# Kernel optimization log

Measured on AMD Instinct MI355X. Metric: run time of the kernel, lower is better.

The kernel has to match this reference:

```python
import jax, jax.numpy as jnp
import numpy as np

B, L, H = 8, 1024, 512
CHUNK = 16  # query-row chunk size for the score computation; L % CHUNK == 0


def setup_inputs() -> dict:
    key = jax.random.key(0)
    ks = jax.random.split(key, 6)
    s = 1.0 / np.sqrt(H)  # torch nn.Linear default init bound
    return {
        "inputs": jax.random.normal(ks[0], (B, L, H), jnp.float32),
        "W1": jax.random.uniform(ks[1], (H, H), jnp.float32, -s, s),
        "b1": jax.random.uniform(ks[2], (H,), jnp.float32, -s, s),
        "W2": jax.random.uniform(ks[3], (H, H), jnp.float32, -s, s),
        "b2": jax.random.uniform(ks[4], (H,), jnp.float32, -s, s),
        # torch: nn.init.normal_(q, mean=-0.02, std=0.02)
        "q": jax.random.normal(ks[5], (H,), jnp.float32) * 0.02 - 0.02,
    }


def _scores(u1, u2, q):
    # u[b,i,j] = tanh(u1[b,i,:] + u2[b,j,:]) . q  -- computed in row-chunks to
    # avoid materializing the full [B,L,L,H] tensor the torch loop implies.
    Bx, Lx, Hx = u1.shape
    n = Lx // CHUNK
    u1c = u1.reshape(Bx, n, CHUNK, Hx).transpose(1, 0, 2, 3)  # [n, B, c, H]

    def step(carry, u1_i):
        t = jnp.tanh(u1_i[:, :, None, :] + u2[:, None, :, :])  # [B, c, L, H]
        return carry, jnp.einsum('bclh,h->bcl', t, q)

    _, s = jax.lax.scan(jax.checkpoint(step), None, u1c)  # [n, B, c, L]
    return s.transpose(1, 0, 2, 3).reshape(Bx, Lx, Lx)


def reference(inputs, W1, b1, W2, b2, q):
    u1 = inputs @ W1.T + b1  # [B, L, H]
    u2 = inputs @ W2.T + b2  # [B, L, H]
    u = _scores(u1, u2, q)   # [B, L, L]
    # relu=False in init, so no relu on u
    a = jax.nn.softmax(u, axis=2)
    h = jnp.einsum('bij,bjh->bih', a, inputs)  # [B, L, H]
    return h, a
```

## Files before the change

kernel.cpp:

```cpp
#include <hip/hip_runtime.h>

typedef _Float16 f16;
typedef _Float16 f16x2 __attribute__((ext_vector_type(2)));
typedef _Float16 f16x4 __attribute__((ext_vector_type(4)));
typedef _Float16 f16x8 __attribute__((ext_vector_type(8)));
typedef float f32x4 __attribute__((ext_vector_type(4)));

#define LOG2E_X2 2.8853900817779268f

__constant__ float D8[8] = {0.543915f, 0.177997f, 0.0652351f, 0.0242575f,
                            0.00903807f, 0.00336823f, 0.00125536f, 0.000467884f};

static __device__ __forceinline__ void gl2lds16(const void* g, void* l) {
  __builtin_amdgcn_global_load_lds((const __attribute__((address_space(1))) void*)g,
                                   (__attribute__((address_space(3))) void*)l, 16, 0, 0);
}


__global__ __launch_bounds__(256) void k_prep_x(const float* __restrict__ X,
                                                f16* __restrict__ Xh, f16* __restrict__ XhT) {
  const int ht = blockIdx.x, it = blockIdx.y, b = blockIdx.z;
  __shared__ f16 Lt[64][72];
  const int t = threadIdx.x;
  const int r = t >> 4, c4 = (t & 15) * 4;
  const float* Xb = X + ((size_t)b * 1024 + it * 64) * 512 + ht * 64;
#pragma unroll
  for (int k = 0; k < 4; ++k) {
    const int rr = r + 16 * k;
    float4 v = *(const float4*)&Xb[(size_t)rr * 512 + c4];
    f16 h0 = (f16)v.x, h1 = (f16)v.y, h2 = (f16)v.z, h3 = (f16)v.w;
    *(f16x4*)&Xh[((size_t)b * 1024 + it * 64 + rr) * 512 + ht * 64 + c4] = {h0, h1, h2, h3};
    Lt[c4 + 0][rr] = h0; Lt[c4 + 1][rr] = h1; Lt[c4 + 2][rr] = h2; Lt[c4 + 3][rr] = h3;
  }
  __syncthreads();
  const int hr = t >> 2, seg = t & 3;
  f16* dst = &XhT[((size_t)b * 512 + ht * 64 + hr) * 1024 + it * 64 + seg * 16];
  *(f16x8*)(dst) = *(const f16x8*)&Lt[hr][seg * 16];
  *(f16x8*)(dst + 8) = *(const f16x8*)&Lt[hr][seg * 16 + 8];
}

__global__ __launch_bounds__(256) void k_prep_w(const float* __restrict__ W1,
                                                const float* __restrict__ W2,
                                                f16* __restrict__ Wh) {
  const int row = blockIdx.x, z = blockIdx.y, t = threadIdx.x;
  const float* W = z ? W2 : W1;
  float2 v = *(const float2*)&W[(size_t)row * 512 + t * 2];
  *(f16x2*)&Wh[(size_t)z * 262144 + (size_t)row * 512 + t * 2] = {(f16)v.x, (f16)v.y};
}

template <int NM>
__global__ __launch_bounds__(256) void k_trig(const float* __restrict__ u1,
                                              const float* __restrict__ u2,
                                              const float* __restrict__ q,
                                              f16* __restrict__ At, f16* __restrict__ Bt,
                                              float* __restrict__ qa, float* __restrict__ qb,
                                              int m0, int wq) {
  const int i = blockIdx.x, t = threadIdx.x;
  const float w = 0.62831853f;
  const float2 a2 = *(const float2*)&u1[(size_t)i * 512 + 2 * t];
  const float2 b2 = *(const float2*)&u2[(size_t)i * 512 + 2 * t];
  const float2 q2 = *(const float2*)&q[2 * t];
  if (wq) {
    float sa = q2.x * a2.x + q2.y * a2.y;
    float sb = q2.x * b2.x + q2.y * b2.y;
#pragma unroll
    for (int o = 1; o < 64; o <<= 1) { sa += __shfl_xor(sa, o); sb += __shfl_xor(sb, o); }
    __shared__ float red[8];
    const int lane = t & 63, widx = t >> 6;
    if (lane == 0) { red[widx] = sa; red[4 + widx] = sb; }
    __syncthreads();
    if (t == 0) qa[i] = red[0] + red[1] + red[2] + red[3];
    if (t == 1) qb[i] = red[4] + red[5] + red[6] + red[7];
  }
  float s1[4], c1[4], sm_[4], cm_[4];
  const float ang[4] = {w * a2.x, w * a2.y, w * b2.x, w * b2.y};
#pragma unroll
  for (int u = 0; u < 4; ++u) {
    __sincosf(ang[u], &s1[u], &c1[u]);
    if (m0 == 1) { sm_[u] = s1[u]; cm_[u] = c1[u]; }
    else __sincosf(m0 * ang[u], &sm_[u], &cm_[u]);
  }
  const size_t ldT = (size_t)NM * 1024;
  f16* Ar = At + (size_t)i * ldT + 2 * t;
  f16* Br = Bt + (size_t)i * ldT + 2 * t;
#pragma unroll
  for (int j = 0; j < NM; ++j) {
    const float dm = D8[m0 - 1 + j];
    const float qdx = q2.x * dm, qdy = q2.y * dm;
    *(f16x2*)(Ar + j * 1024)       = {(f16)(qdx * sm_[0]), (f16)(qdy * sm_[1])};
    *(f16x2*)(Ar + j * 1024 + 512) = {(f16)(qdx * cm_[0]), (f16)(qdy * cm_[1])};
    *(f16x2*)(Br + j * 1024)       = {(f16)cm_[2], (f16)cm_[3]};
    *(f16x2*)(Br + j * 1024 + 512) = {(f16)sm_[2], (f16)sm_[3]};
    if (j + 1 < NM) {
#pragma unroll
      for (int u = 0; u < 4; ++u) {
        const float ns = sm_[u] * c1[u] + cm_[u] * s1[u];
        const float nc = cm_[u] * c1[u] - sm_[u] * s1[u];
        sm_[u] = ns; cm_[u] = nc;
      }
    }
  }
}

template <int MODE, int ACC>
__global__ __launch_bounds__(512, 2) void k_gemm(
    const f16* __restrict__ A, const f16* __restrict__ B, float* __restrict__ C,
    const float* __restrict__ e0, const float* __restrict__ e1,
    int Kloop, int ldAB, long halfA, long halfC) {
  __shared__ alignas(16) char sm[2][2][256 * 64 * 2];
  const int t = threadIdx.x;
  const int nx = blockIdx.x, my = blockIdx.y, z = blockIdx.z;
  const f16* Ab; const f16* Bb; float* Cb; const float* bias = nullptr;
  int ldC;
  if (MODE == 0) {
    Ab = A + (size_t)my * 256 * ldAB;
    Bb = B + (size_t)z * 262144 + (size_t)nx * 256 * ldAB;
    Cb = C + (size_t)z * 4194304 + (size_t)my * 256 * 512 + nx * 256;
    bias = (z ? e1 : e0) + nx * 256;
    ldC = 512;
  } else if (MODE == 1) {
    const int b = z & 7, h = z >> 3;
    Ab = A + ((size_t)(b * 1024 + my * 256)) * ldAB + h * halfA;
    Bb = B + ((size_t)(b * 1024 + nx * 256)) * ldAB + h * halfA;
    Cb = C + h * halfC + ((size_t)(b * 1024 + my * 256)) * 1024 + nx * 256;
    ldC = 1024;
  } else {
    Ab = A + ((size_t)(z * 1024 + my * 256)) * ldAB;
    Bb = B + ((size_t)(z * 512 + nx * 256)) * ldAB;
    Cb = C + (size_t)z * 524288 + (size_t)my * 256 * 512 + nx * 256;
    ldC = 512;
  }
  const int wid = t >> 6, lane = t & 63;
  const int wr = wid >> 2, wc = wid & 3;
  const int rl = lane & 15, kc = lane >> 4;
  f32x4 acc[8][4] = {};

  auto stage = [&](int buf, int kt) {
    const f16* gA = Ab + kt * 64;
    const f16* gB = Bb + kt * 64;
    char* lA = sm[buf][0];
    char* lB = sm[buf][1];
#pragma unroll
    for (int ii = 0; ii < 4; ++ii) {
      const int lin = ii * 512 + t;
      const int row = lin >> 3, c = lin & 7;
      const size_t go = (size_t)row * ldAB + ((c ^ (row & 7)) * 8);
      gl2lds16(gA + go, lA + ii * 8192 + wid * 1024);
      gl2lds16(gB + go, lB + ii * 8192 + wid * 1024);
    }
  };

  const int nkt = Kloop >> 6;
  stage(0, 0);
  __syncthreads();
  for (int kt = 0; kt < nkt; ++kt) {
    const int cur = kt & 1;
    if (kt + 1 < nkt) stage(cur ^ 1, kt + 1);
    const char* lA = sm[cur][0];
    const char* lB = sm[cur][1];
#pragma unroll
    for (int kk = 0; kk < 2; ++kk) {
      f16x8 av[8], bv[4];
#pragma unroll
      for (int fi = 0; fi < 8; ++fi) {
        const int rloc = wr * 128 + fi * 16 + rl;
        av[fi] = *(const f16x8*)(lA + rloc * 128 + (((kc + 4 * kk) ^ (rloc & 7)) << 4));
      }
#pragma unroll
      for (int fj = 0; fj < 4; ++fj) {
        const int cloc = wc * 64 + fj * 16 + rl;
        bv[fj] = *(const f16x8*)(lB + cloc * 128 + (((kc + 4 * kk) ^ (cloc & 7)) << 4));
      }
#pragma unroll
      for (int fi = 0; fi < 8; ++fi)
#pragma unroll
        for (int fj = 0; fj < 4; ++fj)
          acc[fi][fj] = __builtin_amdgcn_mfma_f32_16x16x32_f16(av[fi], bv[fj], acc[fi][fj], 0, 0, 0);
    }
    __syncthreads();
  }
#pragma unroll
  for (int fj = 0; fj < 4; ++fj) {
    const int gcol = wc * 64 + fj * 16 + rl;
    const float bvv = (MODE == 0) ? bias[gcol] : 0.f;
#pragma unroll
    for (int fi = 0; fi < 8; ++fi) {
      const int grow0 = wr * 128 + fi * 16 + kc * 4;
      f32x4 v = acc[fi][fj];
#pragma unroll
      for (int r = 0; r < 4; ++r) {
        const size_t o = (size_t)(grow0 + r) * ldC + gcol;
        float x = v[r] + bvv;
        if (ACC) x += Cb[o];
        Cb[o] = x;
      }
    }
  }
}

__global__ __launch_bounds__(256) void k_softmax2(const float* __restrict__ P0,
                                                  const float* __restrict__ P1,
                                                  const float* __restrict__ qa,
                                                  const float* __restrict__ qb,
                                                  float* __restrict__ out_a,
                                                  f16* __restrict__ a16) {
  const int row = blockIdx.x, t = threadIdx.x;
  const int b = row >> 10;
  const size_t off = (size_t)row * 1024 + t * 4;
  float4 p0 = *(const float4*)(P0 + off);
  float4 p1 = *(const float4*)(P1 + off);
  float4 qb4 = *(const float4*)(qb + (size_t)b * 1024 + t * 4);
  const float qi = qa[row];
  float4 v;
  v.x = p0.x + p1.x + 0.2f * (qi + qb4.x);
  v.y = p0.y + p1.y + 0.2f * (qi + qb4.y);
  v.z = p0.z + p1.z + 0.2f * (qi + qb4.z);
  v.w = p0.w + p1.w + 0.2f * (qi + qb4.w);
  float m = fmaxf(fmaxf(v.x, v.y), fmaxf(v.z, v.w));
#pragma unroll
  for (int o = 1; o < 64; o <<= 1) m = fmaxf(m, __shfl_xor(m, o));
  __shared__ float red[4];
  const int w = t >> 6, ln = t & 63;
  if (ln == 0) red[w] = m;
  __syncthreads();
  m = fmaxf(fmaxf(red[0], red[1]), fmaxf(red[2], red[3]));
  v.x = __expf(v.x - m); v.y = __expf(v.y - m);
  v.z = __expf(v.z - m); v.w = __expf(v.w - m);
  float s = v.x + v.y + v.z + v.w;
#pragma unroll
  for (int o = 1; o < 64; o <<= 1) s += __shfl_xor(s, o);
  __syncthreads();
  if (ln == 0) red[w] = s;
  __syncthreads();
  s = red[0] + red[1] + red[2] + red[3];
  const float inv = 1.0f / s;
  v.x *= inv; v.y *= inv; v.z *= inv; v.w *= inv;
  *(float4*)(out_a + off) = v;
  *(f16x4*)(a16 + off) = {(f16)v.x, (f16)v.y, (f16)v.z, (f16)v.w};
}

typedef short s16x2 __attribute__((ext_vector_type(2)));

static __device__ __forceinline__ float fdot2f(f16x2 a, f16x2 b, float c) {
#if __has_builtin(__builtin_amdgcn_fdot2)
  return __builtin_amdgcn_fdot2(a, b, c, false);
#else
  return c + (float)a[0] * (float)b[0] + (float)a[1] * (float)b[1];
#endif
}

__global__ void k_qprep(const float* __restrict__ q, f16* __restrict__ qh,
                        float* __restrict__ qsum) {
  const int t = threadIdx.x;
  float v = q[t];
  qh[t] = (f16)v;
  float s = v;
#pragma unroll
  for (int o = 1; o < 64; o <<= 1) s += __shfl_xor(s, o);
  __shared__ float red[8];
  if ((t & 63) == 0) red[t >> 6] = s;
  __syncthreads();
  if (t == 0) {
    float tot = 0.f;
#pragma unroll
    for (int i = 0; i < 8; ++i) tot += red[i];
    *qsum = tot;
  }
}

__global__ __launch_bounds__(256) void k_gemm_exp(
    const float* __restrict__ X, const float* __restrict__ W1,
    const float* __restrict__ b1, const float* __restrict__ W2,
    const float* __restrict__ b2, f16* __restrict__ e1, f16* __restrict__ e2) {
  const int z = blockIdx.z;
  const float* W = z ? W2 : W1;
  const float* bias = z ? b2 : b1;
  f16* out = z ? e2 : e1;
  const int r0 = blockIdx.y * 64;
  const int c0 = blockIdx.x * 64;
  __shared__ alignas(16) float Xs[64][68];
  __shared__ alignas(16) float Ws[64][68];
  const int t = threadIdx.x;
  const int row = t >> 2, seg = t & 3;
  const int tr = t >> 4, tc = t & 15;
  float acc[4][4] = {};
#pragma unroll 1
  for (int k0 = 0; k0 < 512; k0 += 64) {
    const float4* gx = (const float4*)(X + (size_t)(r0 + row) * 512 + k0 + seg * 16);
    float4* lx = (float4*)(&Xs[row][seg * 16]);
    lx[0] = gx[0]; lx[1] = gx[1]; lx[2] = gx[2]; lx[3] = gx[3];
    const float4* gw = (const float4*)(W + (size_t)(c0 + row) * 512 + k0 + seg * 16);
    float4* lw = (float4*)(&Ws[row][seg * 16]);
    lw[0] = gw[0]; lw[1] = gw[1]; lw[2] = gw[2]; lw[3] = gw[3];
    __syncthreads();
#pragma unroll 4
    for (int kk = 0; kk < 64; kk += 4) {
      float4 av[4], bv[4];
#pragma unroll
      for (int ii = 0; ii < 4; ++ii) av[ii] = *(const float4*)&Xs[tr + 16 * ii][kk];
#pragma unroll
      for (int jj = 0; jj < 4; ++jj) bv[jj] = *(const float4*)&Ws[tc + 16 * jj][kk];
#pragma unroll
      for (int ii = 0; ii < 4; ++ii) {
#pragma unroll
        for (int jj = 0; jj < 4; ++jj) {
          acc[ii][jj] = fmaf(av[ii].x, bv[jj].x, acc[ii][jj]);
          acc[ii][jj] = fmaf(av[ii].y, bv[jj].y, acc[ii][jj]);
          acc[ii][jj] = fmaf(av[ii].z, bv[jj].z, acc[ii][jj]);
          acc[ii][jj] = fmaf(av[ii].w, bv[jj].w, acc[ii][jj]);
        }
      }
    }
    __syncthreads();
  }
#pragma unroll
  for (int ii = 0; ii < 4; ++ii) {
    const int r = r0 + tr + 16 * ii;
#pragma unroll
    for (int jj = 0; jj < 4; ++jj) {
      const int c = c0 + tc + 16 * jj;
      float u = acc[ii][jj] + bias[c];
      float val = u * LOG2E_X2 - 4.0f;
      val = fminf(6.6759f, fmaxf(-14.6759f, val));
      out[(size_t)r * 512 + c] = (f16)exp2f(val);
    }
  }
}

template <int P>
static __device__ __forceinline__ void tanh_dot_step(const f16x8 (&Av)[4],
                                                     const f16x8 (&Bv)[4],
                                                     const f16x8& Qv, float (&acc)[4][4],
                                                     int c256, int kmag, int two2) {
  f16x2 qp = __builtin_shufflevector(Qv, Qv, 2 * P, 2 * P + 1);
#pragma unroll
  for (int jj = 0; jj < 4; ++jj) {
    f16x2 bp = __builtin_shufflevector(Bv[jj], Bv[jj], 2 * P, 2 * P + 1);
#pragma unroll
    for (int ii = 0; ii < 4; ++ii) {
      f16x2 ap = __builtin_shufflevector(Av[ii], Av[ii], 2 * P, 2 * P + 1);
      f16x2 d, r, tt;
      asm("v_pk_fma_f16 %0, %3, %4, %5\n\t"
          "v_pk_sub_i16 %1, %6, %0\n\t"
          "v_pk_fma_f16 %2, %0, %1, %7 neg_lo:[1,0,0] neg_hi:[1,0,0]\n\t"
          "v_pk_mul_f16 %1, %1, %2\n\t"
          "v_pk_fma_f16 %2, %0, %1, %7 neg_lo:[1,0,0] neg_hi:[1,0,0]\n\t"
          "v_pk_mul_f16 %1, %1, %2"
          : "=&v"(d), "=&v"(r), "=&v"(tt)
          : "v"(ap), "v"(bp), "v"(c256), "v"(kmag), "v"(two2));
      acc[ii][jj] = fdot2f(r, qp, acc[ii][jj]);
    }
  }
}

__global__ __launch_bounds__(256) void k_scores(const f16* __restrict__ e1,
                                                const f16* __restrict__ e2,
                                                const f16* __restrict__ qh,
                                                const float* __restrict__ qsum_p,
                                                float* __restrict__ out_a) {
  const int b = blockIdx.z, it = blockIdx.y, jt = blockIdx.x;
  __shared__ alignas(16) f16 As[64][72];
  __shared__ alignas(16) f16 Bs[64][72];
  __shared__ alignas(16) f16 Qs[512];
  const int t = threadIdx.x;
  const size_t eA = (size_t)(b * 1024 + it * 64) * 512;
  const size_t eB = (size_t)(b * 1024 + jt * 64) * 512;
  if (t < 64) ((uint4*)Qs)[t] = ((const uint4*)qh)[t];
  const int row = t >> 2, seg = t & 3;
  const int tr = t >> 4, tc = t & 15;
  const int c256 = 0x1C001C00;
  const int kmag = 0x77987798;
  const int two2 = 0x40004000;
  float acc[4][4] = {};
#pragma unroll 1
  for (int h0 = 0; h0 < 512; h0 += 64) {
    const f16* gA = e1 + eA + (size_t)row * 512 + h0;
    const f16* gB = e2 + eB + (size_t)row * 512 + h0;
    *(uint4*)(&As[row][seg * 8]) = *(const uint4*)(gA + seg * 8);
    *(uint4*)(&As[row][seg * 8 + 32]) = *(const uint4*)(gA + seg * 8 + 32);
    *(uint4*)(&Bs[row][seg * 8]) = *(const uint4*)(gB + seg * 8);
    *(uint4*)(&Bs[row][seg * 8 + 32]) = *(const uint4*)(gB + seg * 8 + 32);
    __syncthreads();
#pragma unroll 2
    for (int g = 0; g < 8; ++g) {
      f16x8 Av[4], Bv[4], Qv;
#pragma unroll
      for (int ii = 0; ii < 4; ++ii) Av[ii] = *(const f16x8*)&As[tr + 16 * ii][g * 8];
#pragma unroll
      for (int jj = 0; jj < 4; ++jj) Bv[jj] = *(const f16x8*)&Bs[tc + 16 * jj][g * 8];
      Qv = *(const f16x8*)&Qs[h0 + g * 8];
      tanh_dot_step<0>(Av, Bv, Qv, acc, c256, kmag, two2);
      tanh_dot_step<1>(Av, Bv, Qv, acc, c256, kmag, two2);
      tanh_dot_step<2>(Av, Bv, Qv, acc, c256, kmag, two2);
      tanh_dot_step<3>(Av, Bv, Qv, acc, c256, kmag, two2);
    }
    __syncthreads();
  }
  const float qs = *qsum_p;
#pragma unroll
  for (int ii = 0; ii < 4; ++ii) {
    const size_t orow = (size_t)(b * 1024 + it * 64 + tr + 16 * ii) * 1024;
#pragma unroll
    for (int jj = 0; jj < 4; ++jj)
      out_a[orow + jt * 64 + tc + 16 * jj] = qs - acc[ii][jj] * (1.0f / 128.0f);
  }
}

__global__ __launch_bounds__(256) void k_softmax(float* __restrict__ a) {
  float* row = a + (size_t)blockIdx.x * 1024;
  const int t = threadIdx.x;
  float4 v = ((const float4*)row)[t];
  float m = fmaxf(fmaxf(v.x, v.y), fmaxf(v.z, v.w));
#pragma unroll
  for (int o = 1; o < 64; o <<= 1) m = fmaxf(m, __shfl_xor(m, o));
  __shared__ float red[4];
  const int w = t >> 6, ln = t & 63;
  if (ln == 0) red[w] = m;
  __syncthreads();
  m = fmaxf(fmaxf(red[0], red[1]), fmaxf(red[2], red[3]));
  v.x = __expf(v.x - m); v.y = __expf(v.y - m);
  v.z = __expf(v.z - m); v.w = __expf(v.w - m);
  float s = v.x + v.y + v.z + v.w;
#pragma unroll
  for (int o = 1; o < 64; o <<= 1) s += __shfl_xor(s, o);
  __syncthreads();
  if (ln == 0) red[w] = s;
  __syncthreads();
  s = red[0] + red[1] + red[2] + red[3];
  const float inv = 1.0f / s;
  v.x *= inv; v.y *= inv; v.z *= inv; v.w *= inv;
  ((float4*)row)[t] = v;
}

__global__ __launch_bounds__(256) void k_av(const float* __restrict__ a,
                                            const float* __restrict__ X,
                                            float* __restrict__ h) {
  const int b = blockIdx.z;
  const int i0 = blockIdx.y * 64;
  const int c0 = blockIdx.x * 64;
  __shared__ alignas(16) float As[64][68];
  __shared__ alignas(16) float Xs[64][68];
  const float* Ab = a + (size_t)b * 1024 * 1024;
  const float* Xb = X + (size_t)b * 1024 * 512;
  const int t = threadIdx.x;
  const int row = t >> 2, seg = t & 3;
  const int tr = t >> 4, tc = t & 15;
  float acc[4][4] = {};
#pragma unroll 1
  for (int k0 = 0; k0 < 1024; k0 += 64) {
    const float4* ga = (const float4*)(Ab + (size_t)(i0 + row) * 1024 + k0 + seg * 16);
    float4* la = (float4*)(&As[row][seg * 16]);
    la[0] = ga[0]; la[1] = ga[1]; la[2] = ga[2]; la[3] = ga[3];
    const float4* gx = (const float4*)(Xb + (size_t)(k0 + row) * 512 + c0 + seg * 16);
    float4* lx = (float4*)(&Xs[row][seg * 16]);
    lx[0] = gx[0]; lx[1] = gx[1]; lx[2] = gx[2]; lx[3] = gx[3];
    __syncthreads();
#pragma unroll 8
    for (int k = 0; k < 64; ++k) {
      float av[4], bv[4];
#pragma unroll
      for (int ii = 0; ii < 4; ++ii) av[ii] = As[tr + 16 * ii][k];
#pragma unroll
      for (int jj = 0; jj < 4; ++jj) bv[jj] = Xs[k][tc + 16 * jj];
#pragma unroll
      for (int ii = 0; ii < 4; ++ii) {
#pragma unroll
        for (int jj = 0; jj < 4; ++jj)
          acc[ii][jj] = fmaf(av[ii], bv[jj], acc[ii][jj]);
      }
    }
    __syncthreads();
  }
#pragma unroll
  for (int ii = 0; ii < 4; ++ii) {
    const size_t orow = (size_t)b * 1024 * 512 + (size_t)(i0 + tr + 16 * ii) * 512;
#pragma unroll
    for (int jj = 0; jj < 4; ++jj)
      h[orow + c0 + tc + 16 * jj] = acc[ii][jj];
  }
}

extern "C" void kernel_launch(void* const* d_in, const int* in_sizes, int n_in,
                              void* d_out, int out_size, void* d_ws, size_t ws_size,
                              hipStream_t stream) {
  const float* inputs = (const float*)d_in[0];
  const float* W1 = (const float*)d_in[1];
  const float* b1 = (const float*)d_in[2];
  const float* W2 = (const float*)d_in[3];
  const float* b2 = (const float*)d_in[4];
  const float* q = (const float*)d_in[5];

  float* out_h = (float*)d_out;
  float* out_a = out_h + 4194304;

  const size_t FIXED = 101777408ULL;
  const size_t PER_M = 33554432ULL;
  if (ws_size < FIXED + PER_M) {
    char* ws = (char*)d_ws;
    f16* e1 = (f16*)ws;
    f16* e2 = (f16*)(ws + 8388608);
    f16* qh = (f16*)(ws + 16777216);
    float* qsum = (float*)(ws + 16778240);
    k_qprep<<<1, 512, 0, stream>>>(q, qh, qsum);
    k_gemm_exp<<<dim3(8, 128, 2), 256, 0, stream>>>(inputs, W1, b1, W2, b2, e1, e2);
    k_scores<<<dim3(16, 16, 8), 256, 0, stream>>>(e1, e2, qh, qsum, out_a);
    k_softmax<<<8192, 256, 0, stream>>>(out_a);
    k_av<<<dim3(8, 16, 8), 256, 0, stream>>>(out_a, inputs, out_h);
    return;
  }

  int nm = 8;
  while (FIXED + (size_t)nm * PER_M > ws_size) nm >>= 1;

  char* p = (char*)d_ws;
  f16* Xh = (f16*)p;            p += 8388608;
  f16* XhT = (f16*)p;           p += 8388608;
  f16* Wh = (f16*)p;            p += 1048576;
  f16* a16 = (f16*)p;           p += 16777216;
  float* qa = (float*)p;        p += 32768;
  float* qb = (float*)p;        p += 32768;
  float* P0 = (float*)p;        p += 33554432;
  float* P1 = (float*)p;        p += 33554432;
  f16* At = (f16*)p;            p += (size_t)nm * 16777216;
  f16* Bt = (f16*)p;

  float* u1 = out_a;
  float* u2 = out_a + 4194304;

  k_prep_x<<<dim3(8, 16, 8), 256, 0, stream>>>(inputs, Xh, XhT);
  k_prep_w<<<dim3(512, 2), 256, 0, stream>>>(W1, W2, Wh);
  k_gemm<0, 0><<<dim3(2, 32, 2), 512, 0, stream>>>(Xh, Wh, u1, b1, b2, 512, 512, 0, 0);

  const int chunks = 8 / nm;
  for (int cch = 0; cch < chunks; ++cch) {
    const int m0 = cch * nm + 1;
    switch (nm) {
      case 8: k_trig<8><<<8192, 256, 0, stream>>>(u1, u2, q, At, Bt, qa, qb, m0, cch == 0); break;
      case 4: k_trig<4><<<8192, 256, 0, stream>>>(u1, u2, q, At, Bt, qa, qb, m0, cch == 0); break;
      case 2: k_trig<2><<<8192, 256, 0, stream>>>(u1, u2, q, At, Bt, qa, qb, m0, cch == 0); break;
      default: k_trig<1><<<8192, 256, 0, stream>>>(u1, u2, q, At, Bt, qa, qb, m0, cch == 0); break;
    }
    const int Kloop = nm * 512;
    const int ldAB = nm * 1024;
    const long halfA = (long)nm * 512;
    if (cch == 0)
      k_gemm<1, 0><<<dim3(4, 4, 16), 512, 0, stream>>>(At, Bt, P0, nullptr, nullptr,
                                                       Kloop, ldAB, halfA, 8388608L);
    else
      k_gemm<1, 1><<<dim3(4, 4, 16), 512, 0, stream>>>(At, Bt, P0, nullptr, nullptr,
                                                       Kloop, ldAB, halfA, 8388608L);
  }

  k_softmax2<<<8192, 256, 0, stream>>>(P0, P1, qa, qb, out_a, a16);
  k_gemm<2, 0><<<dim3(2, 4, 8), 512, 0, stream>>>(a16, XhT, out_h, nullptr, nullptr,
                                                  1024, 1024, 0, 0);
}
```

Before: 298.6 us.

## Templatize GEMM tiles, fuse projection GEMMs, add XCD-aware block mapping

The GEMM kernel becomes templated on thread count and warp/fragment tiling. The two input projections now run as one GEMM over concatenated weights with a concatenated bias, writing an interleaved u layout, and using smaller 128x256 tiles for more blocks. The score GEMM uses a 1-D grid remapped so that blocks sharing an XCD work on the same batch/half for L2 locality. The final AV GEMM uses smaller 128x128 tiles with 256 threads for more parallelism. This adds a bias-concatenation kernel launch, and k_trig now reads the interleaved u layout.

```diff
diff --git a/kernel.cpp b/kernel.cpp
--- a/kernel.cpp
+++ b/kernel.cpp
@@ -48,17 +48,22 @@
   *(f16x2*)&Wh[(size_t)z * 262144 + (size_t)row * 512 + t * 2] = {(f16)v.x, (f16)v.y};
 }
 
+__global__ void k_prep_b(const float* __restrict__ b1, const float* __restrict__ b2,
+                         float* __restrict__ biasCat) {
+  const int t = blockIdx.x * 256 + threadIdx.x;
+  biasCat[t] = t < 512 ? b1[t] : b2[t - 512];
+}
+
 template <int NM>
-__global__ __launch_bounds__(256) void k_trig(const float* __restrict__ u1,
-                                              const float* __restrict__ u2,
+__global__ __launch_bounds__(256) void k_trig(const float* __restrict__ u,
                                               const float* __restrict__ q,
                                               f16* __restrict__ At, f16* __restrict__ Bt,
                                               float* __restrict__ qa, float* __restrict__ qb,
                                               int m0, int wq) {
   const int i = blockIdx.x, t = threadIdx.x;
   const float w = 0.62831853f;
-  const float2 a2 = *(const float2*)&u1[(size_t)i * 512 + 2 * t];
-  const float2 b2 = *(const float2*)&u2[(size_t)i * 512 + 2 * t];
+  const float2 a2 = *(const float2*)&u[(size_t)i * 1024 + 2 * t];
+  const float2 b2 = *(const float2*)&u[(size_t)i * 1024 + 512 + 2 * t];
   const float2 q2 = *(const float2*)&q[2 * t];
   if (wq) {
     float sa = q2.x * a2.x + q2.y * a2.y;
@@ -75,10 +80,10 @@
   float s1[4], c1[4], sm_[4], cm_[4];
   const float ang[4] = {w * a2.x, w * a2.y, w * b2.x, w * b2.y};
 #pragma unroll
-  for (int u = 0; u < 4; ++u) {
-    __sincosf(ang[u], &s1[u], &c1[u]);
-    if (m0 == 1) { sm_[u] = s1[u]; cm_[u] = c1[u]; }
-    else __sincosf(m0 * ang[u], &sm_[u], &cm_[u]);
+  for (int uu = 0; uu < 4; ++uu) {
+    __sincosf(ang[uu], &s1[uu], &c1[uu]);
+    if (m0 == 1) { sm_[uu] = s1[uu]; cm_[uu] = c1[uu]; }
+    else __sincosf(m0 * ang[uu], &sm_[uu], &cm_[uu]);
   }
   const size_t ldT = (size_t)NM * 1024;
   f16* Ar = At + (size_t)i * ldT + 2 * t;
@@ -93,31 +98,41 @@
     *(f16x2*)(Br + j * 1024 + 512) = {(f16)sm_[2], (f16)sm_[3]};
     if (j + 1 < NM) {
 #pragma unroll
-      for (int u = 0; u < 4; ++u) {
-        const float ns = sm_[u] * c1[u] + cm_[u] * s1[u];
-        const float nc = cm_[u] * c1[u] - sm_[u] * s1[u];
-        sm_[u] = ns; cm_[u] = nc;
+      for (int uu = 0; uu < 4; ++uu) {
+        const float ns = sm_[uu] * c1[uu] + cm_[uu] * s1[uu];
+        const float nc = cm_[uu] * c1[uu] - sm_[uu] * s1[uu];
+        sm_[uu] = ns; cm_[uu] = nc;
       }
     }
   }
 }
 
-template <int MODE, int ACC>
-__global__ __launch_bounds__(512, 2) void k_gemm(
+template <int MODE, int ACC, int T, int WR, int WC, int FI, int FJ>
+__global__ __launch_bounds__(T, 2) void k_gemmG(
     const f16* __restrict__ A, const f16* __restrict__ B, float* __restrict__ C,
-    const float* __restrict__ e0, const float* __restrict__ e1,
-    int Kloop, int ldAB, long halfA, long halfC) {
-  __shared__ alignas(16) char sm[2][2][256 * 64 * 2];
-  const int t = threadIdx.x;
-  const int nx = blockIdx.x, my = blockIdx.y, z = blockIdx.z;
+    const float* __restrict__ bias0, int Kloop, int ldAB, long halfA, long halfC) {
+  constexpr int BM = WR * FI * 16;
+  constexpr int BN = WC * FJ * 16;
+  __shared__ alignas(16) char smA[2][BM * 128];
+  __shared__ alignas(16) char smB[2][BN * 128];
+  const int t = threadIdx.x;
+  int nx, my, z;
+  if (MODE == 1) {
+    const int lin = blockIdx.x;
+    const int xcd = lin & 7, s = lin >> 3;
+    const int g = xcd + 8 * (s >> 2);
+    nx = s & 3; my = g & 3; z = g >> 2;
+  } else {
+    nx = blockIdx.x; my = blockIdx.y; z = blockIdx.z;
+  }
   const f16* Ab; const f16* Bb; float* Cb; const float* bias = nullptr;
   int ldC;
   if (MODE == 0) {
-    Ab = A + (size_t)my * 256 * ldAB;
-    Bb = B + (size_t)z * 262144 + (size_t)nx * 256 * ldAB;
-    Cb = C + (size_t)z * 4194304 + (size_t)my * 256 * 512 + nx * 256;
-    bias = (z ? e1 : e0) + nx * 256;
-    ldC = 512;
+    Ab = A + (size_t)my * BM * ldAB;
+    Bb = B + (size_t)nx * BN * ldAB;
+    Cb = C + (size_t)my * BM * 1024 + nx * BN;
+    bias = bias0 + nx * BN;
+    ldC = 1024;
   } else if (MODE == 1) {
     const int b = z & 7, h = z >> 3;
     Ab = A + ((size_t)(b * 1024 + my * 256)) * ldAB + h * halfA;
@@ -125,28 +140,33 @@
     Cb = C + h * halfC + ((size_t)(b * 1024 + my * 256)) * 1024 + nx * 256;
     ldC = 1024;
   } else {
-    Ab = A + ((size_t)(z * 1024 + my * 256)) * ldAB;
-    Bb = B + ((size_t)(z * 512 + nx * 256)) * ldAB;
-    Cb = C + (size_t)z * 524288 + (size_t)my * 256 * 512 + nx * 256;
+    Ab = A + (size_t)z * 1048576 + (size_t)my * BM * ldAB;
+    Bb = B + (size_t)z * 524288 + (size_t)nx * BN * ldAB;
+    Cb = C + (size_t)z * 524288 + (size_t)my * BM * 512 + nx * BN;
     ldC = 512;
   }
   const int wid = t >> 6, lane = t & 63;
-  const int wr = wid >> 2, wc = wid & 3;
+  const int wr = wid / WC, wc = wid % WC;
   const int rl = lane & 15, kc = lane >> 4;
-  f32x4 acc[8][4] = {};
+  f32x4 acc[FI][FJ] = {};
 
   auto stage = [&](int buf, int kt) {
     const f16* gA = Ab + kt * 64;
     const f16* gB = Bb + kt * 64;
-    char* lA = sm[buf][0];
-    char* lB = sm[buf][1];
-#pragma unroll
-    for (int ii = 0; ii < 4; ++ii) {
-      const int lin = ii * 512 + t;
-      const int row = lin >> 3, c = lin & 7;
-      const size_t go = (size_t)row * ldAB + ((c ^ (row & 7)) * 8);
-      gl2lds16(gA + go, lA + ii * 8192 + wid * 1024);
-      gl2lds16(gB + go, lB + ii * 8192 + wid * 1024);
+    constexpr int LA = BM * 8 / T, LB = BN * 8 / T;
+#pragma unroll
+    for (int ii = 0; ii < LA; ++ii) {
+      const int idx = ii * T + t;
+      const int row = idx >> 3, c = idx & 7;
+      gl2lds16(gA + (size_t)row * ldAB + ((c ^ (row & 7)) * 8),
+               smA[buf] + ii * (T * 16) + wid * 1024);
+    }
+#pragma unroll
+    for (int ii = 0; ii < LB; ++ii) {
+      const int idx = ii * T + t;
+      const int row = idx >> 3, c = idx & 7;
+      gl2lds16(gB + (size_t)row * ldAB + ((c ^ (row & 7)) * 8),
+               smB[buf] + ii * (T * 16) + wid * 1024);
     }
   };
 
@@ -156,36 +176,37 @@
   for (int kt = 0; kt < nkt; ++kt) {
     const int cur = kt & 1;
     if (kt + 1 < nkt) stage(cur ^ 1, kt + 1);
-    const char* lA = sm[cur][0];
-    const char* lB = sm[cur][1];
+    const char* lA = smA[cur];
+    const char* lB = smB[cur];
 #pragma unroll
     for (int kk = 0; kk < 2; ++kk) {
-      f16x8 av[8], bv[4];
-#pragma unroll
-      for (int fi = 0; fi < 8; ++fi) {
-        const int rloc = wr * 128 + fi * 16 + rl;
+      f16x8 av[FI], bv[FJ];
+#pragma unroll
+      for (int fi = 0; fi < FI; ++fi) {
+        const int rloc = (wr * FI + fi) * 16 + rl;
         av[fi] = *(const f16x8*)(lA + rloc * 128 + (((kc + 4 * kk) ^ (rloc & 7)) << 4));
       }
 #pragma unroll
-      for (int fj = 0; fj < 4; ++fj) {
-        const int cloc = wc * 64 + fj * 16 + rl;
+      for (int fj = 0; fj < FJ; ++fj) {
+        const int cloc = (wc * FJ + fj) * 16 + rl;
         bv[fj] = *(const f16x8*)(lB + cloc * 128 + (((kc + 4 * kk) ^ (cloc & 7)) << 4));
       }
 #pragma unroll
-      for (int fi = 0; fi < 8; ++fi)
-#pragma unroll
-        for (int fj = 0; fj < 4; ++fj)
+      for (int fi = 0; fi < FI; ++fi)
+#pragma unroll
+        for (int fj = 0; fj < FJ; ++fj)
           acc[fi][fj] = __builtin_amdgcn_mfma_f32_16x16x32_f16(av[fi], bv[fj], acc[fi][fj], 0, 0, 0);
     }
     __syncthreads();
   }
-#pragma unroll
-  for (int fj = 0; fj < 4; ++fj) {
-    const int gcol = wc * 64 + fj * 16 + rl;
+
+#pragma unroll
+  for (int fj = 0; fj < FJ; ++fj) {
+    const int gcol = (wc * FJ + fj) * 16 + rl;
     const float bvv = (MODE == 0) ? bias[gcol] : 0.f;
 #pragma unroll
-    for (int fi = 0; fi < 8; ++fi) {
-      const int grow0 = wr * 128 + fi * 16 + kc * 4;
+    for (int fi = 0; fi < FI; ++fi) {
+      const int grow0 = (wr * FI + fi) * 16 + kc * 4;
       f32x4 v = acc[fi][fj];
 #pragma unroll
       for (int r = 0; r < 4; ++r) {
@@ -493,7 +514,7 @@
   float* out_h = (float*)d_out;
   float* out_a = out_h + 4194304;
 
-  const size_t FIXED = 101777408ULL;
+  const size_t FIXED = 101781504ULL;
   const size_t PER_M = 33554432ULL;
   if (ws_size < FIXED + PER_M) {
     char* ws = (char*)d_ws;
@@ -519,39 +540,41 @@
   f16* a16 = (f16*)p;           p += 16777216;
   float* qa = (float*)p;        p += 32768;
   float* qb = (float*)p;        p += 32768;
+  float* biasCat = (float*)p;   p += 4096;
   float* P0 = (float*)p;        p += 33554432;
   float* P1 = (float*)p;        p += 33554432;
   f16* At = (f16*)p;            p += (size_t)nm * 16777216;
   f16* Bt = (f16*)p;
 
-  float* u1 = out_a;
-  float* u2 = out_a + 4194304;
+  float* u = out_a;
 
   k_prep_x<<<dim3(8, 16, 8), 256, 0, stream>>>(inputs, Xh, XhT);
   k_prep_w<<<dim3(512, 2), 256, 0, stream>>>(W1, W2, Wh);
-  k_gemm<0, 0><<<dim3(2, 32, 2), 512, 0, stream>>>(Xh, Wh, u1, b1, b2, 512, 512, 0, 0);
+  k_prep_b<<<4, 256, 0, stream>>>(b1, b2, biasCat);
+  k_gemmG<0, 0, 512, 2, 4, 4, 4><<<dim3(4, 64, 1), 512, 0, stream>>>(
+      Xh, Wh, u, biasCat, 512, 512, 0, 0);
 
   const int chunks = 8 / nm;
   for (int cch = 0; cch < chunks; ++cch) {
     const int m0 = cch * nm + 1;
     switch (nm) {
-      case 8: k_trig<8><<<8192, 256, 0, stream>>>(u1, u2, q, At, Bt, qa, qb, m0, cch == 0); break;
-      case 4: k_trig<4><<<8192, 256, 0, stream>>>(u1, u2, q, At, Bt, qa, qb, m0, cch == 0); break;
-      case 2: k_trig<2><<<8192, 256, 0, stream>>>(u1, u2, q, At, Bt, qa, qb, m0, cch == 0); break;
-      default: k_trig<1><<<8192, 256, 0, stream>>>(u1, u2, q, At, Bt, qa, qb, m0, cch == 0); break;
+      case 8: k_trig<8><<<8192, 256, 0, stream>>>(u, q, At, Bt, qa, qb, m0, cch == 0); break;
+      case 4: k_trig<4><<<8192, 256, 0, stream>>>(u, q, At, Bt, qa, qb, m0, cch == 0); break;
+      case 2: k_trig<2><<<8192, 256, 0, stream>>>(u, q, At, Bt, qa, qb, m0, cch == 0); break;
+      default: k_trig<1><<<8192, 256, 0, stream>>>(u, q, At, Bt, qa, qb, m0, cch == 0); break;
     }
     const int Kloop = nm * 512;
     const int ldAB = nm * 1024;
     const long halfA = (long)nm * 512;
     if (cch == 0)
-      k_gemm<1, 0><<<dim3(4, 4, 16), 512, 0, stream>>>(At, Bt, P0, nullptr, nullptr,
-                                                       Kloop, ldAB, halfA, 8388608L);
+      k_gemmG<1, 0, 512, 2, 4, 8, 4><<<dim3(256, 1, 1), 512, 0, stream>>>(
+          At, Bt, P0, nullptr, Kloop, ldAB, halfA, 8388608L);
     else
-      k_gemm<1, 1><<<dim3(4, 4, 16), 512, 0, stream>>>(At, Bt, P0, nullptr, nullptr,
-                                                       Kloop, ldAB, halfA, 8388608L);
+      k_gemmG<1, 1, 512, 2, 4, 8, 4><<<dim3(256, 1, 1), 512, 0, stream>>>(
+          At, Bt, P0, nullptr, Kloop, ldAB, halfA, 8388608L);
   }
 
   k_softmax2<<<8192, 256, 0, stream>>>(P0, P1, qa, qb, out_a, a16);
-  k_gemm<2, 0><<<dim3(2, 4, 8), 512, 0, stream>>>(a16, XhT, out_h, nullptr, nullptr,
-                                                  1024, 1024, 0, 0);
-}
+  k_gemmG<2, 0, 256, 2, 2, 4, 4><<<dim3(4, 8, 8), 256, 0, stream>>>(
+      a16, XhT, out_h, nullptr, 1024, 1024, 0, 0);
+}
```

Result: no change. 295.7 us, median of 2 (-1.0%).
